# Kernel optimization log

Measured on AMD Instinct MI355X. Metric: run time of the kernel, lower is better.

Reference implementation:

```python
import jax, jax.numpy as jnp
import numpy as np

N = 10000; G = 100; NPG = 100; E = 400000; EPG = 4000
C = 32; L = 3; LM = 16; S = 4; NB = 8; NL = 3
CUT = 6.0; AVG = 40.0
L_OF = np.array([0, 1, 1, 1, 2, 2, 2, 2, 2, 3, 3, 3, 3, 3, 3, 3])  # l of each lm slot


def sph_harm(v):
    # component-normalized real spherical harmonics up to l=3 on unit vectors
    x, y, z = v[..., 0], v[..., 1], v[..., 2]
    s3 = jnp.sqrt(3.0); s5 = jnp.sqrt(5.0); s15 = jnp.sqrt(15.0)
    Y = [jnp.ones_like(x),
         s3 * x, s3 * y, s3 * z,
         s15 * x * y, s15 * y * z, 0.5 * s5 * (3 * z * z - 1.0), s15 * x * z, 0.5 * s15 * (x * x - y * y),
         jnp.sqrt(35.0 / 8.0) * y * (3 * x * x - y * y), jnp.sqrt(105.0) * x * y * z,
         jnp.sqrt(21.0 / 8.0) * y * (5 * z * z - 1.0), 0.5 * jnp.sqrt(7.0) * (5 * z ** 3 - 3 * z),
         jnp.sqrt(21.0 / 8.0) * x * (5 * z * z - 1.0), 0.5 * jnp.sqrt(105.0) * z * (x * x - y * y),
         jnp.sqrt(35.0 / 8.0) * x * (x * x - 3 * y * y)]
    return jnp.stack(Y, axis=-1)  # [E, 16]


def bessel_cutoff(r):
    # bessel basis (r_max=1) * polynomial cutoff (p=2)
    n = jnp.arange(1, NB + 1, dtype=r.dtype)
    rs = jnp.where(r > 1e-9, r, 1e-9)
    b = jnp.sqrt(2.0) * jnp.sin(jnp.pi * n[None, :] * rs[:, None]) / rs[:, None]
    f = jnp.where(r < 1.0, 1.0 - 6.0 * r ** 2 + 8.0 * r ** 3 - 3.0 * r ** 4, 0.0)
    return b * f[:, None]  # [E, NB]


def setup_inputs() -> dict:
    key = jax.random.key(0)
    ks = jax.random.split(key, 20)
    positions = jax.random.normal(ks[0], (N, 3), dtype=jnp.float32)
    cell = jnp.eye(3, dtype=jnp.float32)[None] * 3.0 + 0.05 * jax.random.normal(ks[1], (G, 3, 3), dtype=jnp.float32)
    Sij = jax.random.randint(ks[2], (E, 3), 0, 3).astype(jnp.int32) - 1
    gid = jnp.arange(E, dtype=jnp.int32) // EPG
    ia = gid * NPG + jax.random.randint(ks[3], (E,), 0, NPG).astype(jnp.int32)
    ja = gid * NPG + jax.random.randint(ks[4], (E,), 0, NPG).astype(jnp.int32)
    edge_index = jnp.stack([ia, ja], axis=0)
    species = jax.random.randint(ks[5], (N,), 0, S).astype(jnp.int32)
    batch = (jnp.arange(N, dtype=jnp.int32) // NPG)
    sc = 0.1
    return {
        'positions': positions, 'cell': cell, 'Sij': Sij, 'edge_index': edge_index,
        'species': species, 'batch': batch,
        'W_emb': sc * jax.random.normal(ks[6], (S, C), dtype=jnp.float32),
        'W_xtp': sc * jax.random.normal(ks[7], (C, S), dtype=jnp.float32),
        'W_up': sc * jax.random.normal(ks[8], (NL, L + 1, C, C), dtype=jnp.float32),
        'W1': sc * jax.random.normal(ks[9], (NL, NB, 64), dtype=jnp.float32),
        'b1': jnp.zeros((NL, 64), dtype=jnp.float32),
        'W2': sc * jax.random.normal(ks[10], (NL, 64, 64), dtype=jnp.float32),
        'b2': jnp.zeros((NL, 64), dtype=jnp.float32),
        'W3': sc * jax.random.normal(ks[11], (NL, 64, 2 * C * (L + 1)), dtype=jnp.float32),
        'W_down': sc * jax.random.normal(ks[12], (NL, L + 1, C, C), dtype=jnp.float32),
        'W_sc': sc * jax.random.normal(ks[13], (NL, L + 1, C, S, C), dtype=jnp.float32),
        'Wr1': sc * jax.random.normal(ks[14], (NL, C, 64), dtype=jnp.float32),
        'br1': jnp.zeros((NL, 64), dtype=jnp.float32),
        'Wr2': sc * jax.random.normal(ks[15], (NL, 64, 1), dtype=jnp.float32),
    }


def reference(positions, cell, Sij, edge_index, species, batch, W_emb, W_xtp, W_up,
              W1, b1, W2, b2, W3, W_down, W_sc, Wr1, br1, Wr2):
    ia, ja = edge_index[0], edge_index[1]
    eg = batch[ia]  # graph id of each edge
    shift = jnp.einsum('ei,eij->ej', Sij.astype(positions.dtype), cell[eg])
    Rij = (positions[ja] - positions[ia] + shift) / CUT
    r = jnp.linalg.norm(Rij, axis=1)
    u = Rij / jnp.where(r > 1e-9, r, 1e-9)[:, None]
    Y = sph_harm(u)                      # [E, 16]
    ef = bessel_cutoff(r)                # [E, 8]
    attrs = jax.nn.one_hot(species, S, dtype=positions.dtype)
    h0 = attrs @ W_emb                   # node embedding [N, C]
    h = jnp.zeros((N, C, LM), positions.dtype).at[:, :, 0].set(h0)
    xnode = jnp.einsum('nc,ns,cs->n', h0, attrs, W_xtp)  # x_node_tp -> 1x0e
    lof = jnp.asarray(L_OF)
    outs = []
    for layer in range(NL):
        hu = jnp.einsum('ncm,mcd->ndm', h, W_up[layer][lof])  # linear up (per-l)
        hm = jax.nn.silu(ef @ W1[layer] + b1[layer])
        hm = jax.nn.silu(hm @ W2[layer] + b2[layer])
        rw = (hm @ W3[layer]).reshape(-1, 2, C, L + 1)        # per-edge TP weights
        w = rw[:, :, :, lof]                                  # [E, 2, C, 16]
        hj = hu[ja]                                           # gather sender feats
        m = w[:, 0] * Y[:, None, :] * hj[:, :, :1] + w[:, 1] * hj  # depthwise TP paths
        agg = jax.ops.segment_sum(m, ia, num_segments=N) / AVG
        hmsg = jnp.einsum('ncm,mcd->ndm', agg, W_down[layer][lof])
        sc = jnp.einsum('ncm,ns,mcsd->ndm', h, attrs, W_sc[layer][lof])  # self-conn TP
        h = hmsg * xnode[:, None, None] + sc                  # product block
        e = jax.nn.silu(h[:, :, 0] @ Wr1[layer] + br1[layer]) @ Wr2[layer]
        outs.append(e[:, 0])
    node_e = jax.nn.silu(jnp.stack(outs, -1)).sum(-1)
    return jax.ops.segment_sum(node_e, batch, num_segments=G)  # per-graph energy [G]
```

## Files before the change

### kernel.cpp

```cpp
#include <hip/hip_runtime.h>
#include <hip/hip_bf16.h>
#include <hip/hip_fp16.h>
#include <stdint.h>

#define NN   10000
#define GG   100
#define NPG  100
#define EE   400000
#define EPG  4000
#define CC   32
#define LM   16
#define SS   4
#define NBES 8
#define NLAYER 3
#define INV_AVG (1.0f/40.0f)
#define MLPB 6256

typedef _Float16 f16x8 __attribute__((ext_vector_type(8)));
typedef _Float16 f16x4 __attribute__((ext_vector_type(4)));
typedef _Float16 f16x2 __attribute__((ext_vector_type(2)));
typedef float    f32x4 __attribute__((ext_vector_type(4)));

__device__ __forceinline__ float siluf(float x) { return x / (1.0f + __expf(-x)); }
__device__ __forceinline__ int lof(int m) { return (m >= 1) + (m >= 4) + (m >= 9); }
__device__ __forceinline__ f16x2 asf16x2(unsigned u) {
  union { unsigned u; f16x2 f; } x; x.u = u; return x.f;
}

__device__ __forceinline__ void geom_body(
    int e, const float* __restrict__ pos, const float* __restrict__ cell,
    const int* __restrict__ Sij, const int* __restrict__ eidx,
    const int* __restrict__ batch, __half* __restrict__ Y, __half* __restrict__ ef)
{
  int ia = eidx[e], ja = eidx[EE + e];
  int g = batch[ia];
  float s0 = (float)Sij[e*3+0], s1 = (float)Sij[e*3+1], s2 = (float)Sij[e*3+2];
  const float* cg = cell + g*9;
  float shx = s0*cg[0] + s1*cg[3] + s2*cg[6];
  float shy = s0*cg[1] + s1*cg[4] + s2*cg[7];
  float shz = s0*cg[2] + s1*cg[5] + s2*cg[8];
  float rx = (pos[ja*3+0] - pos[ia*3+0] + shx) / 6.0f;
  float ry = (pos[ja*3+1] - pos[ia*3+1] + shy) / 6.0f;
  float rz = (pos[ja*3+2] - pos[ia*3+2] + shz) / 6.0f;
  float r2 = rx*rx + ry*ry + rz*rz;
  float r  = sqrtf(r2);
  float rs = (r > 1e-9f) ? r : 1e-9f;
  float inv = 1.0f / rs;
  float x = rx*inv, y = ry*inv, z = rz*inv;

  const float s3   = 1.7320508075688772f;
  const float s15  = 3.872983346207417f;
  const float s5h  = 1.118033988749895f;
  const float s15h = 1.9364916731037085f;
  const float s358 = 2.091650066335189f;
  const float s105 = 10.246950765959598f;
  const float s218 = 1.620185174601965f;
  const float s7h  = 1.3228756555322954f;
  const float s105h= 5.123475382979799f;

  float xx = x*x, yy = y*y, zz = z*z;
  float yv[16];
  yv[0]  = 1.0f;
  yv[1]  = s3*x;  yv[2] = s3*y;  yv[3] = s3*z;
  yv[4]  = s15*x*y; yv[5] = s15*y*z; yv[6] = s5h*(3.0f*zz - 1.0f);
  yv[7]  = s15*x*z; yv[8] = s15h*(xx - yy);
  yv[9]  = s358*y*(3.0f*xx - yy);
  yv[10] = s105*x*y*z;
  yv[11] = s218*y*(5.0f*zz - 1.0f);
  yv[12] = s7h*(5.0f*zz*z - 3.0f*z);
  yv[13] = s218*x*(5.0f*zz - 1.0f);
  yv[14] = s105h*z*(xx - yy);
  yv[15] = s358*x*(xx - 3.0f*yy);

  union { __half h[16]; uint4 u[2]; } yp;
  #pragma unroll
  for (int i = 0; i < 16; ++i) yp.h[i] = __float2half(yv[i]);
  uint4* Yp = (uint4*)(Y + (size_t)e*16);
  Yp[0] = yp.u[0];
  Yp[1] = yp.u[1];

  float f = 0.0f;
  if (r < 1.0f) f = 1.0f - 6.0f*r2 + 8.0f*r2*r - 3.0f*r2*r2;
  float c1 = 1.4142135623730951f * f * inv;
  float ang = 3.14159265358979323846f * rs;
  float sn = __sinf(ang), cn = __cosf(ang);
  float twoc = 2.0f * cn;
  float sprev = 0.0f, scur = sn;
  union { __half h[8]; uint4 u; } p;
  #pragma unroll
  for (int n1 = 1; n1 <= NBES; ++n1) {
    p.h[n1-1] = __float2half(c1 * scur);
    float snext = twoc * scur - sprev;
    sprev = scur; scur = snext;
  }
  *(uint4*)(ef + (size_t)e*8) = p.u;
}

__global__ __launch_bounds__(256) void k_pre(
    const float* __restrict__ pos, const float* __restrict__ cell,
    const int* __restrict__ Sij, const int* __restrict__ eidx,
    const int* __restrict__ batch, __half* __restrict__ Y, __half* __restrict__ ef,
    const int* __restrict__ species, const float* __restrict__ W_emb,
    const float* __restrict__ W_xtp, float* __restrict__ h,
    float* __restrict__ xnode, float* __restrict__ node_e,
    const float* __restrict__ W2, const float* __restrict__ W3,
    _Float16* __restrict__ W2t, _Float16* __restrict__ W3t,
    int* __restrict__ cnt)
{
  int b = blockIdx.x, t = threadIdx.x;
  if (b < 1563) {
    int e = b*256 + t;
    if (e < EE) geom_body(e, pos, cell, Sij, eidx, batch, Y, ef);
  } else if (b < 2813) {
    int idx = (b - 1563)*256 + t;
    if (idx < NN*CC) {
      int n = idx / CC, c = idx % CC;
      int sp = species[n];
      float h0 = W_emb[sp*CC + c];
      float* hp = h + (size_t)n*512 + c*16;
      hp[0] = h0;
      #pragma unroll
      for (int m = 1; m < 16; ++m) hp[m] = 0.0f;
      if (c == 0) {
        float xn = 0.0f;
        for (int c2 = 0; c2 < CC; ++c2) xn += W_emb[sp*CC + c2] * W_xtp[c2*SS + sp];
        xnode[n] = xn;
        node_e[n] = 0.0f;
      }
    }
  } else if (b < 3005) {
    int idx = (b - 2813)*256 + t;
    if (idx < NLAYER*64*64) {
      int l = idx / 4096, rem = idx % 4096, k = rem / 64, j = rem % 64;
      W2t[l*4096 + j*64 + k] = (_Float16)W2[idx];
    }
    if (idx < NLAYER*64*256) {
      int l = idx / 16384, rem = idx % 16384, k = rem / 256, j = rem % 256;
      W3t[l*16384 + j*64 + k] = (_Float16)W3[idx];
    }
  } else {
    int e = (b - 3005)*256 + t;
    if (e < EE) atomicAdd(&cnt[eidx[e]], 1);
  }
}

__global__ __launch_bounds__(128) void k_csr_scan(
    const int* __restrict__ cnt, int* __restrict__ off, int* __restrict__ cursor) {
  __shared__ int s[128];
  int g = blockIdx.x, t = threadIdx.x;
  int own = (t < NPG) ? cnt[g*NPG + t] : 0;
  s[t] = own;
  __syncthreads();
  #pragma unroll
  for (int d = 1; d < 128; d <<= 1) {
    int v = (t >= d) ? s[t-d] : 0;
    __syncthreads();
    s[t] += v;
    __syncthreads();
  }
  if (t < NPG) {
    int o = g*EPG + s[t] - own;
    off[g*NPG + t] = o;
    cursor[g*NPG + t] = o;
    if (g == GG-1 && t == NPG-1) off[NN] = EE;
  }
}

__global__ __launch_bounds__(256) void k_csr_fill(
    const int* __restrict__ eidx, int* __restrict__ cursor, int2* __restrict__ elist) {
  int e = blockIdx.x * 256 + threadIdx.x;
  if (e >= EE) return;
  int ia = eidx[e], ja = eidx[EE + e];
  int pos = atomicAdd(&cursor[ia], 1);
  elist[pos] = make_int2(e*128, ja*1024);
}

__device__ __forceinline__ void mlp_body(
    int mb, int t, _Float16* pool16,
    const __half* __restrict__ ef, const float* __restrict__ W1,
    const float* __restrict__ b1, const _Float16* __restrict__ W2t,
    const float* __restrict__ b2, __half* __restrict__ hm2)
{
  int eb = (mb & 7) * 782 + (mb >> 3);
  if (eb >= EE/64) return;
  int wv = t >> 6, lane = t & 63;
  int ln15 = lane & 15, quad = lane >> 4;
  _Float16* hm1 = pool16 + wv*(16*72);
  size_t e16 = (size_t)eb*64 + wv*16;

  union { uint4 u; __half hh[8]; } efv;
  efv.u = *(const uint4*)(ef + (e16 + ln15)*8);
  float ev[8];
  #pragma unroll
  for (int k = 0; k < 8; ++k) ev[k] = __half2float(efv.hh[k]);
  #pragma unroll
  for (int p = 0; p < 4; ++p) {
    int j0 = p*16 + quad*4;
    float4 a = *(const float4*)(b1 + j0);
    #pragma unroll
    for (int k = 0; k < 8; ++k) {
      const float4 w = *(const float4*)(W1 + k*64 + j0);
      a.x += ev[k]*w.x; a.y += ev[k]*w.y; a.z += ev[k]*w.z; a.w += ev[k]*w.w;
    }
    f16x4 pk;
    pk[0] = (_Float16)siluf(a.x);
    pk[1] = (_Float16)siluf(a.y);
    pk[2] = (_Float16)siluf(a.z);
    pk[3] = (_Float16)siluf(a.w);
    *(f16x4*)&hm1[ln15*72 + j0] = pk;
  }

  f16x8 a0 = *(const f16x8*)(hm1 + ln15*72 + quad*8);
  f16x8 a1 = *(const f16x8*)(hm1 + ln15*72 + 32 + quad*8);
  #pragma unroll
  for (int cg = 0; cg < 4; ++cg) {
    int col = cg*16 + ln15;
    f32x4 d = {0.f, 0.f, 0.f, 0.f};
    d = __builtin_amdgcn_mfma_f32_16x16x32_f16(a0, *(const f16x8*)(W2t + (size_t)col*64 + quad*8), d, 0, 0, 0);
    d = __builtin_amdgcn_mfma_f32_16x16x32_f16(a1, *(const f16x8*)(W2t + (size_t)col*64 + 32 + quad*8), d, 0, 0, 0);
    float bb = b2[col];
    #pragma unroll
    for (int r = 0; r < 4; ++r)
      hm2[(e16 + quad*4 + r)*64 + col] = __float2half(siluf(d[r] + bb));
  }
}

__global__ __launch_bounds__(256) void k_mlp(
    const __half* __restrict__ ef, const float* __restrict__ W1,
    const float* __restrict__ b1, const _Float16* __restrict__ W2t,
    const float* __restrict__ b2, __half* __restrict__ hm2)
{
  __shared__ _Float16 pool16[4*16*72];
  mlp_body(blockIdx.x, threadIdx.x, pool16, ef, W1, b1, W2t, b2, hm2);
}

__global__ __launch_bounds__(256) void k_humlp(
    const float* __restrict__ h, const float* __restrict__ Wu,
    __half* __restrict__ hu,
    const __half* __restrict__ ef, const float* __restrict__ W1,
    const float* __restrict__ b1, const _Float16* __restrict__ W2t,
    const float* __restrict__ b2, __half* __restrict__ hm2)
{
  __shared__ float pool[1152];
  int b = blockIdx.x, t = threadIdx.x;
  if (b < MLPB) {
    __shared__ _Float16 pool16[4*16*72];
    mlp_body(b, t, pool16, ef, W1, b1, W2t, b2, hm2);
    return;
  }
  int n = b - MLPB;
  float* h_s = pool;
  float* hu_s = pool + 512;
  h_s[t]       = h[(size_t)n*512 + t];
  h_s[t + 256] = h[(size_t)n*512 + t + 256];
  __syncthreads();
  int lane = t & 63, wv = t >> 6;
  int d = lane & 31, ch = lane >> 5;
  #pragma unroll
  for (int mi = 0; mi < 4; ++mi) {
    int m = wv*4 + mi;
    int l = lof(m);
    const float* wu = Wu + l*1024 + d;
    float u = 0.0f;
    #pragma unroll 4
    for (int cc = 0; cc < 16; ++cc) {
      int c = cc + ch*16;
      u += h_s[c*16 + m] * wu[c*32];
    }
    u += __shfl_xor(u, 32);
    if (ch == 0) hu_s[d*16 + m] = u;
  }
  __syncthreads();
  __half2 o;
  o.x = __float2half(hu_s[2*t]);
  o.y = __float2half(hu_s[2*t + 1]);
  *(__half2*)(hu + (size_t)n*512 + 2*t) = o;
}

__global__ __launch_bounds__(256) void k_gather(
    const int2* __restrict__ elist, const int* __restrict__ off,
    const __half* __restrict__ Y, const __half* __restrict__ hm2,
    const _Float16* __restrict__ W3t, const __half* __restrict__ hu_in,
    const int* __restrict__ species, const float* __restrict__ xnode,
    const float* __restrict__ Wd, const float* __restrict__ Wsc,
    const float* __restrict__ Wr1, const float* __restrict__ br1,
    const float* __restrict__ Wr2, float* __restrict__ node_e,
    const float* __restrict__ Wu_next, __half* __restrict__ hu_out,
    float* __restrict__ h, int has_next,
    int do_mlp, const __half* __restrict__ ef,
    const float* __restrict__ W1n, const float* __restrict__ b1n,
    const _Float16* __restrict__ W2tn, const float* __restrict__ b2n,
    __half* __restrict__ hm2_next)
{
  __shared__ float pool[4608];

  int b = blockIdx.x, t = threadIdx.x;
  if (do_mlp) {
    if (b < MLPB) {
      mlp_body(b, t, (_Float16*)pool, ef, W1n, b1n, W2tn, b2n, hm2_next);
      return;
    }
    b -= MLPB;
  }
  _Float16* rw_base = (_Float16*)pool;
  int2* elw_base = (int2*)((char*)pool + 17408);
  float* al_s = pool;
  float* h2_s = pool + 512;

  int n = (b & 7) * (NN/8) + (b >> 3);
  int beg = off[n], deg = off[n+1] - beg;

  int lane = t & 63, wv = t >> 6;
  int ln15 = lane & 15, quad = lane >> 4;
  _Float16* rww = rw_base + wv*(32*68);
  int2* elw = elw_base + wv*32;
  const char* hm2c = (const char*)hm2;
  const char* Yc   = (const char*)Y;
  const char* huc  = (const char*)hu_in;

  float hreg0 = h[(size_t)n*512 + t];
  float hreg1 = h[(size_t)n*512 + t + 256];

  int mq   = lane & 3;
  int cl   = (lane >> 2) & 7;
  int half = lane >> 5;
  int c    = wv*8 + cl;
  int m0q  = mq*4;
  int la0 = lof(m0q),   lb0 = lof(m0q+1);
  int la1 = lof(m0q+2), lb1 = lof(m0q+3);
  unsigned sel0 = (unsigned)(2*la0) | ((unsigned)(2*la0+1)<<8)
                | ((unsigned)(2*lb0)<<16) | ((unsigned)(2*lb0+1)<<24);
  unsigned sel1 = (unsigned)(2*la1) | ((unsigned)(2*la1+1)<<8)
                | ((unsigned)(2*lb1)<<16) | ((unsigned)(2*lb1+1)<<24);
  unsigned huconst = (unsigned)(c*32 + mq*8);
  unsigned yconst  = (unsigned)(mq*8);
  const char* rwb = (const char*)rww + cl*8;

  float acc0 = 0.f, acc1 = 0.f, acc2 = 0.f, acc3 = 0.f;

  int2 el_cur = make_int2(0, 0);
  f16x8 aA0 = {}, aA1 = {}, aB0 = {}, aB1 = {};
  if (deg > 0) {
    int idx = lane < deg ? lane : deg - 1;
    el_cur = elist[beg + idx];
    int eA = __shfl(el_cur.x, ln15);
    aA0 = *(const f16x8*)(hm2c + (unsigned)eA + quad*16);
    aA1 = *(const f16x8*)(hm2c + (unsigned)eA + 64 + quad*16);
    if (deg > 16) {
      int eB = __shfl(el_cur.x, 16 + ln15);
      aB0 = *(const f16x8*)(hm2c + (unsigned)eB + quad*16);
      aB1 = *(const f16x8*)(hm2c + (unsigned)eB + 64 + quad*16);
    }
  }

  auto edge_body = [&](int i_row, f16x2& av0, f16x2& av1) {
    int2 ed = elw[i_row];
    uint2 hj = *(const uint2*)(huc + ((unsigned)ed.y + huconst));
    unsigned hj0b = (unsigned)__builtin_amdgcn_mov_dpp((int)hj.x, 0, 0xf, 0xf, true);
    unsigned hj0s = __builtin_amdgcn_perm(hj0b, hj0b, 0x01000100u);
    uint2 Ymv = *(const uint2*)(Yc + (((unsigned)ed.x >> 2) + yconst));
    uint2 w0q = *(const uint2*)(rwb + i_row*136);
    uint2 w1q = *(const uint2*)(rwb + i_row*136 + 64);
    unsigned w00 = __builtin_amdgcn_perm(w0q.y, w0q.x, sel0);
    unsigned w01 = __builtin_amdgcn_perm(w0q.y, w0q.x, sel1);
    unsigned w10 = __builtin_amdgcn_perm(w1q.y, w1q.x, sel0);
    unsigned w11 = __builtin_amdgcn_perm(w1q.y, w1q.x, sel1);
    f16x2 hj0v = asf16x2(hj0s);
    av0 += asf16x2(w00) * (asf16x2(Ymv.x) * hj0v) + asf16x2(w10) * asf16x2(hj.x);
    av1 += asf16x2(w01) * (asf16x2(Ymv.y) * hj0v) + asf16x2(w11) * asf16x2(hj.y);
  };

  for (int base = 0; base < deg; base += 32) {
    int cnt = min(32, deg - base);
    if (lane < 32) elw[lane] = el_cur;
    bool useB = cnt > 16;

    #pragma unroll
    for (int cg = 0; cg < 4; ++cg) {
      int colg = (cg < 2) ? (wv*32 + cg*16 + ln15)
                          : (128 + wv*32 + (cg-2)*16 + ln15);
      f16x8 w3a = *(const f16x8*)(W3t + (size_t)colg*64 + quad*8);
      f16x8 w3b = *(const f16x8*)(W3t + (size_t)colg*64 + 32 + quad*8);
      f32x4 dA = {0.f, 0.f, 0.f, 0.f};
      dA = __builtin_amdgcn_mfma_f32_16x16x32_f16(w3a, aA0, dA, 0, 0, 0);
      dA = __builtin_amdgcn_mfma_f32_16x16x32_f16(w3b, aA1, dA, 0, 0, 0);
      f16x4 pA;
      #pragma unroll
      for (int r = 0; r < 4; ++r) pA[r] = (_Float16)dA[r];
      *(f16x4*)&rww[ln15*68 + cg*16 + quad*4] = pA;
      if (useB) {
        f32x4 dB = {0.f, 0.f, 0.f, 0.f};
        dB = __builtin_amdgcn_mfma_f32_16x16x32_f16(w3a, aB0, dB, 0, 0, 0);
        dB = __builtin_amdgcn_mfma_f32_16x16x32_f16(w3b, aB1, dB, 0, 0, 0);
        f16x4 pB;
        #pragma unroll
        for (int r = 0; r < 4; ++r) pB[r] = (_Float16)dB[r];
        *(f16x4*)&rww[(16 + ln15)*68 + cg*16 + quad*4] = pB;
      }
    }

    int2 el_nxt = el_cur;
    f16x8 nA0 = aA0, nA1 = aA1, nB0 = aB0, nB1 = aB1;
    if (base + 32 < deg) {
      int idx = base + 32 + lane;
      if (idx >= deg) idx = deg - 1;
      el_nxt = elist[beg + idx];
      int eA = __shfl(el_nxt.x, ln15);
      nA0 = *(const f16x8*)(hm2c + (unsigned)eA + quad*16);
      nA1 = *(const f16x8*)(hm2c + (unsigned)eA + 64 + quad*16);
      if (deg - (base + 32) > 16) {
        int eB = __shfl(el_nxt.x, 16 + ln15);
        nB0 = *(const f16x8*)(hm2c + (unsigned)eB + quad*16);
        nB1 = *(const f16x8*)(hm2c + (unsigned)eB + 64 + quad*16);
      }
    }

    f16x2 av0 = {(_Float16)0.f, (_Float16)0.f};
    f16x2 av1 = {(_Float16)0.f, (_Float16)0.f};
    int nfull = cnt >> 1;
    #pragma unroll 16
    for (int i = 0; i < nfull; ++i) edge_body(2*i + half, av0, av1);
    if (cnt & 1) {
      if (half == 0) edge_body(cnt - 1, av0, av1);
    }
    acc0 += (float)av0[0]; acc1 += (float)av0[1];
    acc2 += (float)av1[0]; acc3 += (float)av1[1];

    el_cur = el_nxt;
    aA0 = nA0; aA1 = nA1; aB0 = nB0; aB1 = nB1;
  }

  acc0 += __shfl_xor(acc0, 32);
  acc1 += __shfl_xor(acc1, 32);
  acc2 += __shfl_xor(acc2, 32);
  acc3 += __shfl_xor(acc3, 32);

  __syncthreads();

  if (half == 0) {
    *(float4*)&al_s[c*16 + m0q] =
        make_float4(acc0*INV_AVG, acc1*INV_AVG, acc2*INV_AVG, acc3*INV_AVG);
  }
  h2_s[t]       = hreg0;
  h2_s[t + 256] = hreg1;
  __syncthreads();

  int sp = species[n];
  float xn = xnode[n];
  int d = lane & 31, ch = lane >> 5;
  #pragma unroll
  for (int mi = 0; mi < 4; ++mi) {
    int m = wv*4 + mi;
    int l = lof(m);
    const float* wd  = Wd  + l*1024 + d;
    const float* wsc = Wsc + l*4096 + sp*32 + d;
    float a = 0.0f, s = 0.0f;
    #pragma unroll 4
    for (int cc = 0; cc < 16; ++cc) {
      int c2 = cc + ch*16;
      a += al_s[c2*16 + m] * wd[c2*32];
      s += h2_s[c2*16 + m] * wsc[c2*128];
    }
    a += __shfl_xor(a, 32);
    s += __shfl_xor(s, 32);
    float hn = a*xn + s;
    if (ch == 0) h2_s[d*16 + m] = hn;
    if (has_next) {
      const float* wu = Wu_next + l*1024 + d;
      float u = 0.0f;
      #pragma unroll 4
      for (int cc = 0; cc < 16; ++cc) {
        int c2 = cc + ch*16;
        u += h2_s[c2*16 + m] * wu[c2*32];
      }
      u += __shfl_xor(u, 32);
      if (ch == 0) al_s[d*16 + m] = u;
    }
  }

  if (t < 64) {
    float pre = br1[t];
    #pragma unroll 4
    for (int cc = 0; cc < CC; ++cc) pre += h2_s[cc*16] * Wr1[cc*64 + t];
    float v = siluf(pre) * Wr2[t];
    #pragma unroll
    for (int off2 = 32; off2 > 0; off2 >>= 1) v += __shfl_down(v, off2);
    if (t == 0) node_e[n] += siluf(v);
  }
  __syncthreads();

  h[(size_t)n*512 + t]       = h2_s[t];
  h[(size_t)n*512 + t + 256] = h2_s[t + 256];
  if (has_next) {
    __half2 o;
    o.x = __float2half(al_s[2*t]);
    o.y = __float2half(al_s[2*t + 1]);
    *(__half2*)(hu_out + (size_t)n*512 + 2*t) = o;
  }
}

__global__ __launch_bounds__(128) void k_out(
    const float* __restrict__ node_e, float* __restrict__ out)
{
  int g = blockIdx.x, t = threadIdx.x;
  float v = (t < NPG) ? node_e[g*NPG + t] : 0.0f;
  #pragma unroll
  for (int off2 = 32; off2 > 0; off2 >>= 1) v += __shfl_down(v, off2);
  __shared__ float r2[2];
  if ((t & 63) == 0) r2[t >> 6] = v;
  __syncthreads();
  if (t == 0) out[g] = r2[0] + r2[1];
}

__global__ void k_dbg(float* __restrict__ out, float v) {
  int i = blockIdx.x * 64 + threadIdx.x;
  if (i < GG) out[i] = v;
}

extern "C" void kernel_launch(void* const* d_in, const int* in_sizes, int n_in,
                              void* d_out, int out_size, void* d_ws, size_t ws_size,
                              hipStream_t stream)
{
  const float* positions = (const float*)d_in[0];
  const float* cell      = (const float*)d_in[1];
  const int*   Sij       = (const int*)d_in[2];
  const int*   eidx      = (const int*)d_in[3];
  const int*   species   = (const int*)d_in[4];
  const int*   batch     = (const int*)d_in[5];
  const float* W_emb     = (const float*)d_in[6];
  const float* W_xtp     = (const float*)d_in[7];
  const float* W_up      = (const float*)d_in[8];
  const float* W1        = (const float*)d_in[9];
  const float* b1        = (const float*)d_in[10];
  const float* W2        = (const float*)d_in[11];
  const float* b2        = (const float*)d_in[12];
  const float* W3        = (const float*)d_in[13];
  const float* W_down    = (const float*)d_in[14];
  const float* W_sc      = (const float*)d_in[15];
  const float* Wr1       = (const float*)d_in[16];
  const float* br1       = (const float*)d_in[17];
  const float* Wr2       = (const float*)d_in[18];
  float* out = (float*)d_out;
  (void)in_sizes; (void)n_in; (void)out_size;

  const size_t NEED_BASE  = 120000000;
  const size_t NEED_FUSED = 166500000;
  if (ws_size < NEED_BASE) {
    k_dbg<<<dim3(2), dim3(64), 0, stream>>>(out, (float)(ws_size >> 20));
    return;
  }
  const bool fused = ws_size >= NEED_FUSED;

  char* ws = (char*)d_ws;
  size_t off = 0;
  auto alloc = [&](size_t bytes) -> void* {
    void* p = ws + off;
    off += (bytes + 255) & ~(size_t)255;
    return p;
  };
  __half*    Yb      = (__half*)alloc((size_t)EE*16*2);
  __half*    efb     = (__half*)alloc((size_t)EE*8*2);
  float*     hb      = (float*)alloc((size_t)NN*512*4);
  __half*    huA     = (__half*)alloc((size_t)NN*512*2);
  __half*    huB     = (__half*)alloc((size_t)NN*512*2);
  float*     xnodeb  = (float*)alloc((size_t)NN*4);
  float*     node_eb = (float*)alloc((size_t)NN*4);
  int*       offb    = (int*)alloc((size_t)(NN+1)*4);
  int*       curb    = (int*)alloc((size_t)NN*4);
  int2*      elistb  = (int2*)alloc((size_t)EE*8);
  _Float16*  W2tb    = (_Float16*)alloc((size_t)NLAYER*64*64*2);
  _Float16*  W3tb    = (_Float16*)alloc((size_t)NLAYER*64*256*2);
  __half*    hm2A    = (__half*)alloc((size_t)EE*64*2);
  __half*    hm2B    = fused ? (__half*)alloc((size_t)EE*64*2) : hm2A;

  dim3 blk(256);
  hipMemsetAsync(curb, 0, (size_t)NN*4, stream);
  k_pre<<<dim3(4568), blk, 0, stream>>>(positions, cell, Sij, eidx, batch,
      Yb, efb, species, W_emb, W_xtp, hb, xnodeb, node_eb,
      W2, W3, W2tb, W3tb, curb);
  k_csr_scan<<<dim3(GG), dim3(128), 0, stream>>>(curb, offb, curb);
  k_csr_fill<<<dim3((EE + 255)/256), blk, 0, stream>>>(eidx, curb, elistb);

  k_humlp<<<dim3(MLPB + NN), blk, 0, stream>>>(hb, W_up + 0*4096, huA,
      efb, W1 + 0, b1 + 0, W2tb + 0, b2 + 0, hm2A);

  __half* hin = huA; __half* hout = huB;
  __half* hm2_cur = hm2A; __half* hm2_nxt = hm2B;
  for (int layer = 0; layer < NLAYER; ++layer) {
    int has_next = (layer + 1 < NLAYER) ? 1 : 0;
    int do_mlp = (fused && has_next) ? 1 : 0;
    int nl = has_next ? layer + 1 : 0;
    k_gather<<<dim3(NN + (do_mlp ? MLPB : 0)), blk, 0, stream>>>(
        elistb, offb, Yb, hm2_cur,
        W3tb + layer*16384, hin,
        species, xnodeb,
        W_down + layer*4096, W_sc + layer*16384,
        Wr1 + layer*CC*64, br1 + layer*64, Wr2 + layer*64, node_eb,
        W_up + (has_next ? (layer+1)*4096 : 0), hout, hb, has_next,
        do_mlp, efb,
        W1 + nl*NBES*64, b1 + nl*64, W2tb + nl*4096, b2 + nl*64,
        hm2_nxt);
    if (!fused && has_next) {
      k_mlp<<<dim3(MLPB), blk, 0, stream>>>(efb,
          W1 + (layer+1)*NBES*64, b1 + (layer+1)*64,
          W2tb + (layer+1)*4096, b2 + (layer+1)*64, hm2A);
    }
    __half* tmp = hin; hin = hout; hout = tmp;
    if (fused) { __half* t2 = hm2_cur; hm2_cur = hm2_nxt; hm2_nxt = t2; }
  }
  k_out<<<dim3(GG), dim3(128), 0, stream>>>(node_eb, out);
}
```

Before: 948.3 us.

## Prefetch edge indices and gathered features in register batches in k_gather

```diff
diff --git a/kernel.cpp b/kernel.cpp
--- a/kernel.cpp
+++ b/kernel.cpp
@@ -277,7 +277,7 @@
   *(__half2*)(hu + (size_t)n*512 + 2*t) = o;
 }
 
-__global__ __launch_bounds__(256) void k_gather(
+__global__ __launch_bounds__(256, 3) void k_gather(
     const int2* __restrict__ elist, const int* __restrict__ off,
     const __half* __restrict__ Y, const __half* __restrict__ hm2,
     const _Float16* __restrict__ W3t, const __half* __restrict__ hu_in,
@@ -292,7 +292,7 @@
     const _Float16* __restrict__ W2tn, const float* __restrict__ b2n,
     __half* __restrict__ hm2_next)
 {
-  __shared__ float pool[4608];
+  __shared__ float pool[4352];
 
   int b = blockIdx.x, t = threadIdx.x;
   if (do_mlp) {
@@ -303,7 +303,6 @@
     b -= MLPB;
   }
   _Float16* rw_base = (_Float16*)pool;
-  int2* elw_base = (int2*)((char*)pool + 17408);
   float* al_s = pool;
   float* h2_s = pool + 512;
 
@@ -313,7 +312,6 @@
   int lane = t & 63, wv = t >> 6;
   int ln15 = lane & 15, quad = lane >> 4;
   _Float16* rww = rw_base + wv*(32*68);
-  int2* elw = elw_base + wv*32;
   const char* hm2c = (const char*)hm2;
   const char* Yc   = (const char*)Y;
   const char* huc  = (const char*)hu_in;
@@ -334,7 +332,16 @@
                 | ((unsigned)(2*lb1)<<16) | ((unsigned)(2*lb1+1)<<24);
   unsigned huconst = (unsigned)(c*32 + mq*8);
   unsigned yconst  = (unsigned)(mq*8);
-  const char* rwb = (const char*)rww + cl*8;
+  const char* rwbh = (const char*)rww + cl*8 + half*136;
+
+  f16x8 w3A[4], w3B[4];
+  #pragma unroll
+  for (int cg = 0; cg < 4; ++cg) {
+    int colg = (cg < 2) ? (wv*32 + cg*16 + ln15)
+                        : (128 + wv*32 + (cg-2)*16 + ln15);
+    w3A[cg] = *(const f16x8*)(W3t + (size_t)colg*64 + quad*8);
+    w3B[cg] = *(const f16x8*)(W3t + (size_t)colg*64 + 32 + quad*8);
+  }
 
   float acc0 = 0.f, acc1 = 0.f, acc2 = 0.f, acc3 = 0.f;
 
@@ -353,49 +360,71 @@
     }
   }
 
-  auto edge_body = [&](int i_row, f16x2& av0, f16x2& av1) {
-    int2 ed = elw[i_row];
-    uint2 hj = *(const uint2*)(huc + ((unsigned)ed.y + huconst));
+  auto edge_compute = [&](int i, uint2 hj, uint2 Ymv, bool valid,
+                          f16x2& av0, f16x2& av1) {
     unsigned hj0b = (unsigned)__builtin_amdgcn_mov_dpp((int)hj.x, 0, 0xf, 0xf, true);
     unsigned hj0s = __builtin_amdgcn_perm(hj0b, hj0b, 0x01000100u);
-    uint2 Ymv = *(const uint2*)(Yc + (((unsigned)ed.x >> 2) + yconst));
-    uint2 w0q = *(const uint2*)(rwb + i_row*136);
-    uint2 w1q = *(const uint2*)(rwb + i_row*136 + 64);
+    uint2 w0q = *(const uint2*)(rwbh + i*272);
+    uint2 w1q = *(const uint2*)(rwbh + i*272 + 64);
     unsigned w00 = __builtin_amdgcn_perm(w0q.y, w0q.x, sel0);
     unsigned w01 = __builtin_amdgcn_perm(w0q.y, w0q.x, sel1);
     unsigned w10 = __builtin_amdgcn_perm(w1q.y, w1q.x, sel0);
     unsigned w11 = __builtin_amdgcn_perm(w1q.y, w1q.x, sel1);
     f16x2 hj0v = asf16x2(hj0s);
-    av0 += asf16x2(w00) * (asf16x2(Ymv.x) * hj0v) + asf16x2(w10) * asf16x2(hj.x);
-    av1 += asf16x2(w01) * (asf16x2(Ymv.y) * hj0v) + asf16x2(w11) * asf16x2(hj.y);
+    f16x2 c0 = asf16x2(w00) * (asf16x2(Ymv.x) * hj0v) + asf16x2(w10) * asf16x2(hj.x);
+    f16x2 c1 = asf16x2(w01) * (asf16x2(Ymv.y) * hj0v) + asf16x2(w11) * asf16x2(hj.y);
+    if (valid) { av0 += c0; av1 += c1; }
   };
 
   for (int base = 0; base < deg; base += 32) {
     int cnt = min(32, deg - base);
-    if (lane < 32) elw[lane] = el_cur;
     bool useB = cnt > 16;
 
+    int2 ed0[8], ed1[8];
+    #pragma unroll
+    for (int i = 0; i < 8; ++i) {
+      if (2*i < cnt) {
+        int idx = base + 2*i + half;
+        if (idx >= deg) idx = deg - 1;
+        ed0[i] = elist[beg + idx];
+      }
+    }
+    #pragma unroll
+    for (int i = 0; i < 8; ++i) {
+      int ii = 8 + i;
+      if (2*ii < cnt) {
+        int idx = base + 2*ii + half;
+        if (idx >= deg) idx = deg - 1;
+        ed1[i] = elist[beg + idx];
+      }
+    }
+
     #pragma unroll
     for (int cg = 0; cg < 4; ++cg) {
-      int colg = (cg < 2) ? (wv*32 + cg*16 + ln15)
-                          : (128 + wv*32 + (cg-2)*16 + ln15);
-      f16x8 w3a = *(const f16x8*)(W3t + (size_t)colg*64 + quad*8);
-      f16x8 w3b = *(const f16x8*)(W3t + (size_t)colg*64 + 32 + quad*8);
       f32x4 dA = {0.f, 0.f, 0.f, 0.f};
-      dA = __builtin_amdgcn_mfma_f32_16x16x32_f16(w3a, aA0, dA, 0, 0, 0);
-      dA = __builtin_amdgcn_mfma_f32_16x16x32_f16(w3b, aA1, dA, 0, 0, 0);
+      dA = __builtin_amdgcn_mfma_f32_16x16x32_f16(w3A[cg], aA0, dA, 0, 0, 0);
+      dA = __builtin_amdgcn_mfma_f32_16x16x32_f16(w3B[cg], aA1, dA, 0, 0, 0);
       f16x4 pA;
       #pragma unroll
       for (int r = 0; r < 4; ++r) pA[r] = (_Float16)dA[r];
       *(f16x4*)&rww[ln15*68 + cg*16 + quad*4] = pA;
       if (useB) {
         f32x4 dB = {0.f, 0.f, 0.f, 0.f};
-        dB = __builtin_amdgcn_mfma_f32_16x16x32_f16(w3a, aB0, dB, 0, 0, 0);
-        dB = __builtin_amdgcn_mfma_f32_16x16x32_f16(w3b, aB1, dB, 0, 0, 0);
+        dB = __builtin_amdgcn_mfma_f32_16x16x32_f16(w3A[cg], aB0, dB, 0, 0, 0);
+        dB = __builtin_amdgcn_mfma_f32_16x16x32_f16(w3B[cg], aB1, dB, 0, 0, 0);
         f16x4 pB;
         #pragma unroll
         for (int r = 0; r < 4; ++r) pB[r] = (_Float16)dB[r];
         *(f16x4*)&rww[(16 + ln15)*68 + cg*16 + quad*4] = pB;
+      }
+    }
+
+    uint2 hjA[8], ymA[8];
+    #pragma unroll
+    for (int i = 0; i < 8; ++i) {
+      if (2*i < cnt) {
+        hjA[i] = *(const uint2*)(huc + ((unsigned)ed0[i].y + huconst));
+        ymA[i] = *(const uint2*)(Yc + (((unsigned)ed0[i].x >> 2) + yconst));
       }
     }
 
@@ -417,12 +446,33 @@
 
     f16x2 av0 = {(_Float16)0.f, (_Float16)0.f};
     f16x2 av1 = {(_Float16)0.f, (_Float16)0.f};
-    int nfull = cnt >> 1;
-    #pragma unroll 16
-    for (int i = 0; i < nfull; ++i) edge_body(2*i + half, av0, av1);
-    if (cnt & 1) {
-      if (half == 0) edge_body(cnt - 1, av0, av1);
-    }
+    #pragma unroll
+    for (int i = 0; i < 8; ++i) {
+      if (2*i < cnt) {
+        bool valid = (2*i + half) < cnt;
+        edge_compute(i, hjA[i], ymA[i], valid, av0, av1);
+      }
+    }
+
+    uint2 hjB[8], ymB[8];
+    #pragma unroll
+    for (int i = 0; i < 8; ++i) {
+      int ii = 8 + i;
+      if (2*ii < cnt) {
+        hjB[i] = *(const uint2*)(huc + ((unsigned)ed1[i].y + huconst));
+        ymB[i] = *(const uint2*)(Yc + (((unsigned)ed1[i].x >> 2) + yconst));
+      }
+    }
+
+    #pragma unroll
+    for (int i = 0; i < 8; ++i) {
+      int ii = 8 + i;
+      if (2*ii < cnt) {
+        bool valid = (2*ii + half) < cnt;
+        edge_compute(ii, hjB[i], ymB[i], valid, av0, av1);
+      }
+    }
+
     acc0 += (float)av0[0]; acc1 += (float)av0[1];
     acc2 += (float)av1[0]; acc3 += (float)av1[1];
 
```

New measurement: 1.188 ms. +25.3%, slower.

## Stage sender features and Y rows in LDS via async global-to-LDS loads

Applied to the files above, without the earlier changes.

```diff
diff --git a/kernel.cpp b/kernel.cpp
--- a/kernel.cpp
+++ b/kernel.cpp
@@ -25,6 +25,12 @@
 __device__ __forceinline__ int lof(int m) { return (m >= 1) + (m >= 4) + (m >= 9); }
 __device__ __forceinline__ f16x2 asf16x2(unsigned u) {
   union { unsigned u; f16x2 f; } x; x.u = u; return x.f;
+}
+
+__device__ __forceinline__ void gload_lds16(const void* g, void* l) {
+  __builtin_amdgcn_global_load_lds(
+      (const __attribute__((address_space(1))) unsigned int*)g,
+      (__attribute__((address_space(3))) unsigned int*)l, 16, 0, 0);
 }
 
 __device__ __forceinline__ void geom_body(
@@ -292,7 +298,7 @@
     const _Float16* __restrict__ W2tn, const float* __restrict__ b2n,
     __half* __restrict__ hm2_next)
 {
-  __shared__ float pool[4608];
+  __shared__ float pool[13056];
 
   int b = blockIdx.x, t = threadIdx.x;
   if (do_mlp) {
@@ -303,7 +309,8 @@
     b -= MLPB;
   }
   _Float16* rw_base = (_Float16*)pool;
-  int2* elw_base = (int2*)((char*)pool + 17408);
+  char* hu_sc = (char*)pool + 17408;
+  char* Ys_c  = (char*)pool + 51200;
   float* al_s = pool;
   float* h2_s = pool + 512;
 
@@ -313,7 +320,7 @@
   int lane = t & 63, wv = t >> 6;
   int ln15 = lane & 15, quad = lane >> 4;
   _Float16* rww = rw_base + wv*(32*68);
-  int2* elw = elw_base + wv*32;
+  const char* rwc = (const char*)rww;
   const char* hm2c = (const char*)hm2;
   const char* Yc   = (const char*)Y;
   const char* huc  = (const char*)hu_in;
@@ -333,8 +340,15 @@
   unsigned sel1 = (unsigned)(2*la1) | ((unsigned)(2*la1+1)<<8)
                 | ((unsigned)(2*lb1)<<16) | ((unsigned)(2*lb1+1)<<24);
   unsigned huconst = (unsigned)(c*32 + mq*8);
-  unsigned yconst  = (unsigned)(mq*8);
-  const char* rwb = (const char*)rww + cl*8;
+
+  f16x8 w3A[4], w3B[4];
+  #pragma unroll
+  for (int cg = 0; cg < 4; ++cg) {
+    int colg = (cg < 2) ? (wv*32 + cg*16 + ln15)
+                        : (128 + wv*32 + (cg-2)*16 + ln15);
+    w3A[cg] = *(const f16x8*)(W3t + (size_t)colg*64 + quad*8);
+    w3B[cg] = *(const f16x8*)(W3t + (size_t)colg*64 + 32 + quad*8);
+  }
 
   float acc0 = 0.f, acc1 = 0.f, acc2 = 0.f, acc3 = 0.f;
 
@@ -353,14 +367,13 @@
     }
   }
 
-  auto edge_body = [&](int i_row, f16x2& av0, f16x2& av1) {
-    int2 ed = elw[i_row];
-    uint2 hj = *(const uint2*)(huc + ((unsigned)ed.y + huconst));
+  auto edge_compute = [&](int s, f16x2& av0, f16x2& av1) {
+    uint2 hj = *(const uint2*)(hu_sc + (unsigned)s*1056 + huconst);
     unsigned hj0b = (unsigned)__builtin_amdgcn_mov_dpp((int)hj.x, 0, 0xf, 0xf, true);
     unsigned hj0s = __builtin_amdgcn_perm(hj0b, hj0b, 0x01000100u);
-    uint2 Ymv = *(const uint2*)(Yc + (((unsigned)ed.x >> 2) + yconst));
-    uint2 w0q = *(const uint2*)(rwb + i_row*136);
-    uint2 w1q = *(const uint2*)(rwb + i_row*136 + 64);
+    uint2 Ymv = *(const uint2*)(Ys_c + (unsigned)s*32 + mq*8);
+    uint2 w0q = *(const uint2*)(rwc + (unsigned)s*136 + cl*8);
+    uint2 w1q = *(const uint2*)(rwc + (unsigned)s*136 + cl*8 + 64);
     unsigned w00 = __builtin_amdgcn_perm(w0q.y, w0q.x, sel0);
     unsigned w01 = __builtin_amdgcn_perm(w0q.y, w0q.x, sel1);
     unsigned w10 = __builtin_amdgcn_perm(w1q.y, w1q.x, sel0);
@@ -372,26 +385,36 @@
 
   for (int base = 0; base < deg; base += 32) {
     int cnt = min(32, deg - base);
-    if (lane < 32) elw[lane] = el_cur;
     bool useB = cnt > 16;
+
+    if (base > 0) __syncthreads();
+
+    #pragma unroll
+    for (int q = 0; q < 8; ++q) {
+      int s = wv*8 + q;
+      if (s < cnt) {
+        int rowoff = __shfl(el_cur.y, s);
+        gload_lds16(huc + (unsigned)rowoff + lane*16, hu_sc + s*1056);
+      }
+    }
+    if (wv == 0) {
+      int yoff = __shfl(el_cur.x, lane >> 1) >> 2;
+      gload_lds16(Yc + (unsigned)yoff + (lane & 1)*16, Ys_c);
+    }
 
     #pragma unroll
     for (int cg = 0; cg < 4; ++cg) {
-      int colg = (cg < 2) ? (wv*32 + cg*16 + ln15)
-                          : (128 + wv*32 + (cg-2)*16 + ln15);
-      f16x8 w3a = *(const f16x8*)(W3t + (size_t)colg*64 + quad*8);
-      f16x8 w3b = *(const f16x8*)(W3t + (size_t)colg*64 + 32 + quad*8);
       f32x4 dA = {0.f, 0.f, 0.f, 0.f};
-      dA = __builtin_amdgcn_mfma_f32_16x16x32_f16(w3a, aA0, dA, 0, 0, 0);
-      dA = __builtin_amdgcn_mfma_f32_16x16x32_f16(w3b, aA1, dA, 0, 0, 0);
+      dA = __builtin_amdgcn_mfma_f32_16x16x32_f16(w3A[cg], aA0, dA, 0, 0, 0);
+      dA = __builtin_amdgcn_mfma_f32_16x16x32_f16(w3B[cg], aA1, dA, 0, 0, 0);
       f16x4 pA;
       #pragma unroll
       for (int r = 0; r < 4; ++r) pA[r] = (_Float16)dA[r];
       *(f16x4*)&rww[ln15*68 + cg*16 + quad*4] = pA;
       if (useB) {
         f32x4 dB = {0.f, 0.f, 0.f, 0.f};
-        dB = __builtin_amdgcn_mfma_f32_16x16x32_f16(w3a, aB0, dB, 0, 0, 0);
-        dB = __builtin_amdgcn_mfma_f32_16x16x32_f16(w3b, aB1, dB, 0, 0, 0);
+        dB = __builtin_amdgcn_mfma_f32_16x16x32_f16(w3A[cg], aB0, dB, 0, 0, 0);
+        dB = __builtin_amdgcn_mfma_f32_16x16x32_f16(w3B[cg], aB1, dB, 0, 0, 0);
         f16x4 pB;
         #pragma unroll
         for (int r = 0; r < 4; ++r) pB[r] = (_Float16)dB[r];
@@ -415,14 +438,14 @@
       }
     }
 
+    __syncthreads();
+
     f16x2 av0 = {(_Float16)0.f, (_Float16)0.f};
     f16x2 av1 = {(_Float16)0.f, (_Float16)0.f};
     int nfull = cnt >> 1;
-    #pragma unroll 16
-    for (int i = 0; i < nfull; ++i) edge_body(2*i + half, av0, av1);
-    if (cnt & 1) {
-      if (half == 0) edge_body(cnt - 1, av0, av1);
-    }
+    #pragma unroll 8
+    for (int i = 0; i < nfull; ++i) edge_compute(2*i + half, av0, av1);
+    if ((cnt & 1) && half == 0) edge_compute(cnt - 1, av0, av1);
     acc0 += (float)av0[0]; acc1 += (float)av0[1];
     acc2 += (float)av1[0]; acc3 += (float)av1[1];
 
```

Result: faster. 925.7 us (-2.4%).

## Make gather kernel persistent over five nodes per block

Applied to the files above, without the earlier changes.

```diff
diff --git a/kernel.cpp b/kernel.cpp
--- a/kernel.cpp
+++ b/kernel.cpp
@@ -15,6 +15,8 @@
 #define NLAYER 3
 #define INV_AVG (1.0f/40.0f)
 #define MLPB 6256
+#define GB   2000
+#define NPB  5
 
 typedef _Float16 f16x8 __attribute__((ext_vector_type(8)));
 typedef _Float16 f16x4 __attribute__((ext_vector_type(4)));
@@ -307,9 +309,6 @@
   float* al_s = pool;
   float* h2_s = pool + 512;
 
-  int n = (b & 7) * (NN/8) + (b >> 3);
-  int beg = off[n], deg = off[n+1] - beg;
-
   int lane = t & 63, wv = t >> 6;
   int ln15 = lane & 15, quad = lane >> 4;
   _Float16* rww = rw_base + wv*(32*68);
@@ -317,9 +316,6 @@
   const char* hm2c = (const char*)hm2;
   const char* Yc   = (const char*)Y;
   const char* huc  = (const char*)hu_in;
-
-  float hreg0 = h[(size_t)n*512 + t];
-  float hreg1 = h[(size_t)n*512 + t + 256];
 
   int mq   = lane & 3;
   int cl   = (lane >> 2) & 7;
@@ -335,167 +331,177 @@
   unsigned huconst = (unsigned)(c*32 + mq*8);
   unsigned yconst  = (unsigned)(mq*8);
   const char* rwb = (const char*)rww + cl*8;
-
-  float acc0 = 0.f, acc1 = 0.f, acc2 = 0.f, acc3 = 0.f;
-
-  int2 el_cur = make_int2(0, 0);
-  f16x8 aA0 = {}, aA1 = {}, aB0 = {}, aB1 = {};
-  if (deg > 0) {
-    int idx = lane < deg ? lane : deg - 1;
-    el_cur = elist[beg + idx];
-    int eA = __shfl(el_cur.x, ln15);
-    aA0 = *(const f16x8*)(hm2c + (unsigned)eA + quad*16);
-    aA1 = *(const f16x8*)(hm2c + (unsigned)eA + 64 + quad*16);
-    if (deg > 16) {
+  int d = lane & 31, ch = lane >> 5;
+
+  for (int it = 0; it < NPB; ++it) {
+    int u = it*GB + b;
+    int n = (u & 7) * (NN/8) + (u >> 3);
+    int beg = off[n], deg = off[n+1] - beg;
+
+    float hreg0 = h[(size_t)n*512 + t];
+    float hreg1 = h[(size_t)n*512 + t + 256];
+
+    float acc0 = 0.0f, acc1 = 0.0f, acc2 = 0.0f, acc3 = 0.0f;
+
+    int2 el_cur = make_int2(0, 0);
+    f16x8 aA0 = {}, aA1 = {}, aB0 = {}, aB1 = {};
+    if (deg > 0) {
+      int idx = lane < deg ? lane : deg - 1;
+      el_cur = elist[beg + idx];
+      int eA = __shfl(el_cur.x, ln15);
       int eB = __shfl(el_cur.x, 16 + ln15);
-      aB0 = *(const f16x8*)(hm2c + (unsigned)eB + quad*16);
-      aB1 = *(const f16x8*)(hm2c + (unsigned)eB + 64 + quad*16);
-    }
-  }
-
-  auto edge_body = [&](int i_row, f16x2& av0, f16x2& av1) {
-    int2 ed = elw[i_row];
-    uint2 hj = *(const uint2*)(huc + ((unsigned)ed.y + huconst));
-    unsigned hj0b = (unsigned)__builtin_amdgcn_mov_dpp((int)hj.x, 0, 0xf, 0xf, true);
-    unsigned hj0s = __builtin_amdgcn_perm(hj0b, hj0b, 0x01000100u);
-    uint2 Ymv = *(const uint2*)(Yc + (((unsigned)ed.x >> 2) + yconst));
-    uint2 w0q = *(const uint2*)(rwb + i_row*136);
-    uint2 w1q = *(const uint2*)(rwb + i_row*136 + 64);
-    unsigned w00 = __builtin_amdgcn_perm(w0q.y, w0q.x, sel0);
-    unsigned w01 = __builtin_amdgcn_perm(w0q.y, w0q.x, sel1);
-    unsigned w10 = __builtin_amdgcn_perm(w1q.y, w1q.x, sel0);
-    unsigned w11 = __builtin_amdgcn_perm(w1q.y, w1q.x, sel1);
-    f16x2 hj0v = asf16x2(hj0s);
-    av0 += asf16x2(w00) * (asf16x2(Ymv.x) * hj0v) + asf16x2(w10) * asf16x2(hj.x);
-    av1 += asf16x2(w01) * (asf16x2(Ymv.y) * hj0v) + asf16x2(w11) * asf16x2(hj.y);
-  };
-
-  for (int base = 0; base < deg; base += 32) {
-    int cnt = min(32, deg - base);
-    if (lane < 32) elw[lane] = el_cur;
-    bool useB = cnt > 16;
-
+      aA0 = *(const f16x8*)(hm2c + (unsigned)eA + quad*16);
+      aA1 = *(const f16x8*)(hm2c + (unsigned)eA + 64 + quad*16);
+      if (deg > 16) {
+        aB0 = *(const f16x8*)(hm2c + (unsigned)eB + quad*16);
+        aB1 = *(const f16x8*)(hm2c + (unsigned)eB + 64 + quad*16);
+      }
+    }
+
+    auto edge_body = [&](int i_row, f16x2& av0, f16x2& av1) {
+      int2 ed = elw[i_row];
+      uint2 hj = *(const uint2*)(huc + ((unsigned)ed.y + huconst));
+      unsigned hj0b = (unsigned)__builtin_amdgcn_mov_dpp((int)hj.x, 0, 0xf, 0xf, true);
+      unsigned hj0s = __builtin_amdgcn_perm(hj0b, hj0b, 0x01000100u);
+      uint2 Ymv = *(const uint2*)(Yc + (((unsigned)ed.x >> 2) + yconst));
+      uint2 w0q = *(const uint2*)(rwb + i_row*136);
+      uint2 w1q = *(const uint2*)(rwb + i_row*136 + 64);
+      unsigned w00 = __builtin_amdgcn_perm(w0q.y, w0q.x, sel0);
+      unsigned w01 = __builtin_amdgcn_perm(w0q.y, w0q.x, sel1);
+      unsigned w10 = __builtin_amdgcn_perm(w1q.y, w1q.x, sel0);
+      unsigned w11 = __builtin_amdgcn_perm(w1q.y, w1q.x, sel1);
+      f16x2 hj0v = asf16x2(hj0s);
+      av0 += asf16x2(w00) * (asf16x2(Ymv.x) * hj0v) + asf16x2(w10) * asf16x2(hj.x);
+      av1 += asf16x2(w01) * (asf16x2(Ymv.y) * hj0v) + asf16x2(w11) * asf16x2(hj.y);
+    };
+
+    for (int base = 0; base < deg; base += 32) {
+      int cnt = min(32, deg - base);
+      if (lane < 32) elw[lane] = el_cur;
+      bool useB = cnt > 16;
+
+      #pragma unroll
+      for (int cg = 0; cg < 4; ++cg) {
+        int colg = (cg < 2) ? (wv*32 + cg*16 + ln15)
+                            : (128 + wv*32 + (cg-2)*16 + ln15);
+        f16x8 b0 = *(const f16x8*)(W3t + (size_t)colg*64 + quad*8);
+        f16x8 b1v = *(const f16x8*)(W3t + (size_t)colg*64 + 32 + quad*8);
+        f32x4 dA = {0.f, 0.f, 0.f, 0.f};
+        dA = __builtin_amdgcn_mfma_f32_16x16x32_f16(b0, aA0, dA, 0, 0, 0);
+        dA = __builtin_amdgcn_mfma_f32_16x16x32_f16(b1v, aA1, dA, 0, 0, 0);
+        f16x4 pA;
+        #pragma unroll
+        for (int r = 0; r < 4; ++r) pA[r] = (_Float16)dA[r];
+        *(f16x4*)&rww[ln15*68 + cg*16 + quad*4] = pA;
+        if (useB) {
+          f32x4 dB = {0.f, 0.f, 0.f, 0.f};
+          dB = __builtin_amdgcn_mfma_f32_16x16x32_f16(b0, aB0, dB, 0, 0, 0);
+          dB = __builtin_amdgcn_mfma_f32_16x16x32_f16(b1v, aB1, dB, 0, 0, 0);
+          f16x4 pB;
+          #pragma unroll
+          for (int r = 0; r < 4; ++r) pB[r] = (_Float16)dB[r];
+          *(f16x4*)&rww[(16 + ln15)*68 + cg*16 + quad*4] = pB;
+        }
+      }
+
+      int2 el_nxt = el_cur;
+      f16x8 nA0 = aA0, nA1 = aA1, nB0 = aB0, nB1 = aB1;
+      if (base + 32 < deg) {
+        int idx = base + 32 + lane;
+        if (idx >= deg) idx = deg - 1;
+        el_nxt = elist[beg + idx];
+        int eA = __shfl(el_nxt.x, ln15);
+        nA0 = *(const f16x8*)(hm2c + (unsigned)eA + quad*16);
+        nA1 = *(const f16x8*)(hm2c + (unsigned)eA + 64 + quad*16);
+        if (deg - (base + 32) > 16) {
+          int eB = __shfl(el_nxt.x, 16 + ln15);
+          nB0 = *(const f16x8*)(hm2c + (unsigned)eB + quad*16);
+          nB1 = *(const f16x8*)(hm2c + (unsigned)eB + 64 + quad*16);
+        }
+      }
+
+      f16x2 av0 = {(_Float16)0.f, (_Float16)0.f};
+      f16x2 av1 = {(_Float16)0.f, (_Float16)0.f};
+      int nfull = cnt >> 1;
+      #pragma unroll 16
+      for (int i = 0; i < nfull; ++i) edge_body(2*i + half, av0, av1);
+      if (cnt & 1) {
+        if (half == 0) edge_body(cnt - 1, av0, av1);
+      }
+      acc0 += (float)av0[0]; acc1 += (float)av0[1];
+      acc2 += (float)av1[0]; acc3 += (float)av1[1];
+
+      el_cur = el_nxt;
+      aA0 = nA0; aA1 = nA1; aB0 = nB0; aB1 = nB1;
+    }
+
+    acc0 += __shfl_xor(acc0, 32);
+    acc1 += __shfl_xor(acc1, 32);
+    acc2 += __shfl_xor(acc2, 32);
+    acc3 += __shfl_xor(acc3, 32);
+
+    __syncthreads();
+
+    if (half == 0) {
+      *(float4*)&al_s[c*16 + m0q] =
+          make_float4(acc0*INV_AVG, acc1*INV_AVG, acc2*INV_AVG, acc3*INV_AVG);
+    }
+    h2_s[t]       = hreg0;
+    h2_s[t + 256] = hreg1;
+    __syncthreads();
+
+    int sp = species[n];
+    float xn = xnode[n];
     #pragma unroll
-    for (int cg = 0; cg < 4; ++cg) {
-      int colg = (cg < 2) ? (wv*32 + cg*16 + ln15)
-                          : (128 + wv*32 + (cg-2)*16 + ln15);
-      f16x8 w3a = *(const f16x8*)(W3t + (size_t)colg*64 + quad*8);
-      f16x8 w3b = *(const f16x8*)(W3t + (size_t)colg*64 + 32 + quad*8);
-      f32x4 dA = {0.f, 0.f, 0.f, 0.f};
-      dA = __builtin_amdgcn_mfma_f32_16x16x32_f16(w3a, aA0, dA, 0, 0, 0);
-      dA = __builtin_amdgcn_mfma_f32_16x16x32_f16(w3b, aA1, dA, 0, 0, 0);
-      f16x4 pA;
-      #pragma unroll
-      for (int r = 0; r < 4; ++r) pA[r] = (_Float16)dA[r];
-      *(f16x4*)&rww[ln15*68 + cg*16 + quad*4] = pA;
-      if (useB) {
-        f32x4 dB = {0.f, 0.f, 0.f, 0.f};
-        dB = __builtin_amdgcn_mfma_f32_16x16x32_f16(w3a, aB0, dB, 0, 0, 0);
-        dB = __builtin_amdgcn_mfma_f32_16x16x32_f16(w3b, aB1, dB, 0, 0, 0);
-        f16x4 pB;
-        #pragma unroll
-        for (int r = 0; r < 4; ++r) pB[r] = (_Float16)dB[r];
-        *(f16x4*)&rww[(16 + ln15)*68 + cg*16 + quad*4] = pB;
-      }
-    }
-
-    int2 el_nxt = el_cur;
-    f16x8 nA0 = aA0, nA1 = aA1, nB0 = aB0, nB1 = aB1;
-    if (base + 32 < deg) {
-      int idx = base + 32 + lane;
-      if (idx >= deg) idx = deg - 1;
-      el_nxt = elist[beg + idx];
-      int eA = __shfl(el_nxt.x, ln15);
-      nA0 = *(const f16x8*)(hm2c + (unsigned)eA + quad*16);
-      nA1 = *(const f16x8*)(hm2c + (unsigned)eA + 64 + quad*16);
-      if (deg - (base + 32) > 16) {
-        int eB = __shfl(el_nxt.x, 16 + ln15);
-        nB0 = *(const f16x8*)(hm2c + (unsigned)eB + quad*16);
-        nB1 = *(const f16x8*)(hm2c + (unsigned)eB + 64 + quad*16);
-      }
-    }
-
-    f16x2 av0 = {(_Float16)0.f, (_Float16)0.f};
-    f16x2 av1 = {(_Float16)0.f, (_Float16)0.f};
-    int nfull = cnt >> 1;
-    #pragma unroll 16
-    for (int i = 0; i < nfull; ++i) edge_body(2*i + half, av0, av1);
-    if (cnt & 1) {
-      if (half == 0) edge_body(cnt - 1, av0, av1);
-    }
-    acc0 += (float)av0[0]; acc1 += (float)av0[1];
-    acc2 += (float)av1[0]; acc3 += (float)av1[1];
-
-    el_cur = el_nxt;
-    aA0 = nA0; aA1 = nA1; aB0 = nB0; aB1 = nB1;
-  }
-
-  acc0 += __shfl_xor(acc0, 32);
-  acc1 += __shfl_xor(acc1, 32);
-  acc2 += __shfl_xor(acc2, 32);
-  acc3 += __shfl_xor(acc3, 32);
-
-  __syncthreads();
-
-  if (half == 0) {
-    *(float4*)&al_s[c*16 + m0q] =
-        make_float4(acc0*INV_AVG, acc1*INV_AVG, acc2*INV_AVG, acc3*INV_AVG);
-  }
-  h2_s[t]       = hreg0;
-  h2_s[t + 256] = hreg1;
-  __syncthreads();
-
-  int sp = species[n];
-  float xn = xnode[n];
-  int d = lane & 31, ch = lane >> 5;
-  #pragma unroll
-  for (int mi = 0; mi < 4; ++mi) {
-    int m = wv*4 + mi;
-    int l = lof(m);
-    const float* wd  = Wd  + l*1024 + d;
-    const float* wsc = Wsc + l*4096 + sp*32 + d;
-    float a = 0.0f, s = 0.0f;
-    #pragma unroll 4
-    for (int cc = 0; cc < 16; ++cc) {
-      int c2 = cc + ch*16;
-      a += al_s[c2*16 + m] * wd[c2*32];
-      s += h2_s[c2*16 + m] * wsc[c2*128];
-    }
-    a += __shfl_xor(a, 32);
-    s += __shfl_xor(s, 32);
-    float hn = a*xn + s;
-    if (ch == 0) h2_s[d*16 + m] = hn;
-    if (has_next) {
-      const float* wu = Wu_next + l*1024 + d;
-      float u = 0.0f;
+    for (int mi = 0; mi < 4; ++mi) {
+      int m = wv*4 + mi;
+      int l = lof(m);
+      const float* wd  = Wd  + l*1024 + d;
+      const float* wsc = Wsc + l*4096 + sp*32 + d;
+      float a = 0.0f, s = 0.0f;
       #pragma unroll 4
       for (int cc = 0; cc < 16; ++cc) {
         int c2 = cc + ch*16;
-        u += h2_s[c2*16 + m] * wu[c2*32];
+        a += al_s[c2*16 + m] * wd[c2*32];
+        s += h2_s[c2*16 + m] * wsc[c2*128];
       }
-      u += __shfl_xor(u, 32);
-      if (ch == 0) al_s[d*16 + m] = u;
-    }
-  }
-
-  if (t < 64) {
-    float pre = br1[t];
-    #pragma unroll 4
-    for (int cc = 0; cc < CC; ++cc) pre += h2_s[cc*16] * Wr1[cc*64 + t];
-    float v = siluf(pre) * Wr2[t];
-    #pragma unroll
-    for (int off2 = 32; off2 > 0; off2 >>= 1) v += __shfl_down(v, off2);
-    if (t == 0) node_e[n] += siluf(v);
-  }
-  __syncthreads();
-
-  h[(size_t)n*512 + t]       = h2_s[t];
-  h[(size_t)n*512 + t + 256] = h2_s[t + 256];
-  if (has_next) {
-    __half2 o;
-    o.x = __float2half(al_s[2*t]);
-    o.y = __float2half(al_s[2*t + 1]);
-    *(__half2*)(hu_out + (size_t)n*512 + 2*t) = o;
+      a += __shfl_xor(a, 32);
+      s += __shfl_xor(s, 32);
+      float hn = a*xn + s;
+      if (ch == 0) h2_s[d*16 + m] = hn;
+      if (has_next) {
+        const float* wu = Wu_next + l*1024 + d;
+        float uacc = 0.0f;
+        #pragma unroll 4
+        for (int cc = 0; cc < 16; ++cc) {
+          int c2 = cc + ch*16;
+          uacc += h2_s[c2*16 + m] * wu[c2*32];
+        }
+        uacc += __shfl_xor(uacc, 32);
+        if (ch == 0) al_s[d*16 + m] = uacc;
+      }
+    }
+
+    if (t < 64) {
+      float pre = br1[t];
+      #pragma unroll 4
+      for (int cc = 0; cc < CC; ++cc) pre += h2_s[cc*16] * Wr1[cc*64 + t];
+      float v = siluf(pre) * Wr2[t];
+      #pragma unroll
+      for (int off2 = 32; off2 > 0; off2 >>= 1) v += __shfl_down(v, off2);
+      if (t == 0) node_e[n] += siluf(v);
+    }
+    __syncthreads();
+
+    h[(size_t)n*512 + t]       = h2_s[t];
+    h[(size_t)n*512 + t + 256] = h2_s[t + 256];
+    if (has_next) {
+      __half2 o;
+      o.x = __float2half(al_s[2*t]);
+      o.y = __float2half(al_s[2*t + 1]);
+      *(__half2*)(hu_out + (size_t)n*512 + 2*t) = o;
+    }
+    __syncthreads();
   }
 }
 
@@ -590,7 +596,7 @@
     int has_next = (layer + 1 < NLAYER) ? 1 : 0;
     int do_mlp = (fused && has_next) ? 1 : 0;
     int nl = has_next ? layer + 1 : 0;
-    k_gather<<<dim3(NN + (do_mlp ? MLPB : 0)), blk, 0, stream>>>(
+    k_gather<<<dim3(GB + (do_mlp ? MLPB : 0)), blk, 0, stream>>>(
         elistb, offb, Yb, hm2_cur,
         W3tb + layer*16384, hin,
         species, xnodeb,
```

Measured after the change: 1.120 ms. +18.1%, slower.
